# Kernel tuning notes

Measured on AMD Instinct MI355X. Metric: run time of the kernel, lower is better.

The kernel has to match this reference:

```python
import jax, jax.numpy as jnp
import numpy as np

N = 50000       # num nodes
E = 400000      # num edges (before self loops)
IN, HID, H, OUT = 128, 64, 4, 64
SLOPE = 0.2     # PyG GATv2Conv default negative_slope


def setup_inputs() -> dict:
    key = jax.random.key(0)
    ks = jax.random.split(key, 14)
    def lin(k, fan_in, fan_out):
        return jax.random.normal(k, (fan_in, fan_out), jnp.float32) / np.sqrt(fan_in)
    return {
        "x": jax.random.normal(ks[0], (N, IN), jnp.float32),
        "edge_index": jax.random.randint(ks[1], (2, E), 0, N, jnp.int32),
        # layer 1: in=IN -> HID per head, H heads, concat
        "Wl1": lin(ks[2], IN, H * HID), "bl1": jnp.zeros((H * HID,), jnp.float32),
        "Wr1": lin(ks[3], IN, H * HID), "br1": jnp.zeros((H * HID,), jnp.float32),
        "att1": jax.random.normal(ks[4], (H, HID), jnp.float32) / np.sqrt(HID),
        "bias1": jnp.zeros((H * HID,), jnp.float32),
        # layer 2: in=H*HID -> OUT, 1 head, concat=False
        "Wl2": lin(ks[5], H * HID, OUT), "bl2": jnp.zeros((OUT,), jnp.float32),
        "Wr2": lin(ks[6], H * HID, OUT), "br2": jnp.zeros((OUT,), jnp.float32),
        "att2": jax.random.normal(ks[7], (1, OUT), jnp.float32) / np.sqrt(OUT),
        "bias2": jnp.zeros((OUT,), jnp.float32),
    }


def gatv2_conv(x, src, dst, Wl, bl, Wr, br, att, heads, out_ch, num_nodes):
    """PyG GATv2Conv (share_weights=False). src->dst aggregation at dst."""
    xl = (x @ Wl + bl).reshape(-1, heads, out_ch)  # source transform (x_j)
    xr = (x @ Wr + br).reshape(-1, heads, out_ch)  # target transform (x_i)
    m = xl[src] + xr[dst]                          # [E, H, C]
    e = jnp.sum(jax.nn.leaky_relu(m, SLOPE) * att, axis=-1)  # [E, H]
    # segment softmax over incoming edges of each dst node
    emax = jax.ops.segment_max(e, dst, num_segments=num_nodes)
    ex = jnp.exp(e - emax[dst])
    denom = jax.ops.segment_sum(ex, dst, num_segments=num_nodes)
    alpha = ex / denom[dst]                        # [E, H]
    out = jax.ops.segment_sum(alpha[:, :, None] * xl[src], dst, num_segments=num_nodes)
    return out  # [N, H, C]


def reference(x, edge_index, Wl1, bl1, Wr1, br1, att1, bias1,
              Wl2, bl2, Wr2, br2, att2, bias2):
    n = x.shape[0]
    loops = jnp.arange(n, dtype=edge_index.dtype)
    src = jnp.concatenate([edge_index[0], loops])  # add_self_loops=True
    dst = jnp.concatenate([edge_index[1], loops])
    h = gatv2_conv(x, src, dst, Wl1, bl1, Wr1, br1, att1, H, HID, n)
    h = h.reshape(n, H * HID) + bias1              # concat=True
    h = jax.nn.elu(h)                              # dropout=0.0
    o = gatv2_conv(h, src, dst, Wl2, bl2, Wr2, br2, att2, 1, OUT, n)
    return o.reshape(n, OUT) + bias2               # concat=False, heads=1
```

## Files before the change

### kernel.cpp

```cpp
#include <hip/hip_runtime.h>
#include <hip/hip_bf16.h>

typedef unsigned short u16;
typedef __attribute__((ext_vector_type(8))) short short8;
typedef __attribute__((ext_vector_type(4))) float floatx4;

#define N_NODES 50000
#define N_EDGES 400000
#define ET      450000
#define F_IN    128
#define C1      256
#define HID     64
#define OUTC    64
#define SLOPE   0.2f

__device__ __forceinline__ float bf2f(u16 v) {
    return __uint_as_float(((unsigned)v) << 16);
}
__device__ __forceinline__ u16 f2bf(float f) {
    unsigned u = __float_as_uint(f);
    return (u16)((u + 0x7fffu + ((u >> 16) & 1u)) >> 16);
}

__global__ __launch_bounds__(256) void detect_kernel(const unsigned* __restrict__ xw,
                                                     int* __restrict__ cnt)
{
    unsigned w = xw[threadIdx.x];
    unsigned aexp = (w >> 7) & 0xFFu;
    if (aexp >= 170u || aexp <= 40u) atomicAdd(cnt, 1);
}

__global__ __launch_bounds__(256) void convert_all_kernel(
    const void* wl1, const void* wr1, const void* wl2, const void* wr2,
    const void* s0, const void* s1, const void* s2, const void* s3,
    const void* s4, const void* s5, const void* s6, const void* s7,
    u16* __restrict__ wt, u16* __restrict__ prm, const int* __restrict__ cnt)
{
    bool f32m = (*cnt >= 32);
    if (blockIdx.x == 384) {
        for (int t = threadIdx.x; t < 1280; t += 256) {
            const void* src; int local;
            if      (t < 256)  { src = s0; local = t; }
            else if (t < 512)  { src = s1; local = t - 256; }
            else if (t < 768)  { src = s2; local = t - 512; }
            else if (t < 1024) { src = s3; local = t - 768; }
            else if (t < 1088) { src = s4; local = t - 1024; }
            else if (t < 1152) { src = s5; local = t - 1088; }
            else if (t < 1216) { src = s6; local = t - 1152; }
            else               { src = s7; local = t - 1216; }
            prm[t] = f32m ? f2bf(((const float*)src)[local]) : ((const u16*)src)[local];
        }
        return;
    }
    int t = blockIdx.x * 256 + threadIdx.x;
    const void* src; int local, k, n, K, base;
    if (t < 32768)      { src = wl1; local = t;         k = local >> 8; n = local & 255; K = 128; base = 0; }
    else if (t < 65536) { src = wr1; local = t - 32768; k = local >> 8; n = local & 255; K = 128; base = 32768; }
    else if (t < 81920) { src = wl2; local = t - 65536; k = local >> 6; n = local & 63;  K = 256; base = 65536; }
    else                { src = wr2; local = t - 81920; k = local >> 6; n = local & 63;  K = 256; base = 81920; }
    u16 v = f32m ? f2bf(((const float*)src)[local]) : ((const u16*)src)[local];
    wt[base + n * K + k] = v;
}

__global__ __launch_bounds__(256) void hist_kernel(const int* __restrict__ ei,
                                                   int* __restrict__ hist)
{
    int t = blockIdx.x * 256 + threadIdx.x;
    if (t >= ET) return;
    int d = (t < N_EDGES) ? ei[N_EDGES + t] : t - N_EDGES;
    atomicAdd(&hist[d], 1);
}

__global__ __launch_bounds__(256) void scan1_kernel(const int* __restrict__ hist,
                                                    int* __restrict__ rowptr,
                                                    int* __restrict__ bsum)
{
    int t = threadIdx.x;
    int i = blockIdx.x * 256 + t;
    int v = (i < N_NODES) ? hist[i] : 0;
    __shared__ int sd[256];
    sd[t] = v;
    __syncthreads();
    #pragma unroll
    for (int ofs = 1; ofs < 256; ofs <<= 1) {
        int u = (t >= ofs) ? sd[t - ofs] : 0;
        __syncthreads();
        sd[t] += u;
        __syncthreads();
    }
    if (i < N_NODES) rowptr[i] = sd[t] - v;
    if (t == 255) bsum[blockIdx.x] = sd[255];
}

__global__ __launch_bounds__(256) void scan2_kernel(int* __restrict__ bsum,
                                                    int* __restrict__ boff)
{
    int t = threadIdx.x;
    int v = (t < 196) ? bsum[t] : 0;
    __shared__ int sd[256];
    sd[t] = v;
    __syncthreads();
    #pragma unroll
    for (int ofs = 1; ofs < 256; ofs <<= 1) {
        int u = (t >= ofs) ? sd[t - ofs] : 0;
        __syncthreads();
        sd[t] += u;
        __syncthreads();
    }
    if (t < 196) boff[t] = sd[t] - v;
}

__global__ __launch_bounds__(256) void scan3_kernel(int* __restrict__ rowptr,
                                                    const int* __restrict__ boff,
                                                    int* __restrict__ off)
{
    int i = blockIdx.x * 256 + threadIdx.x;
    if (i >= N_NODES) return;
    int r = rowptr[i] + boff[blockIdx.x];
    rowptr[i] = r;
    off[i] = r;
}

__global__ __launch_bounds__(256) void scatter_kernel(const int* __restrict__ ei,
                                                      int* __restrict__ off,
                                                      int* __restrict__ src_csr)
{
    int t = blockIdx.x * 256 + threadIdx.x;
    if (t >= ET) return;
    int s, d;
    if (t < N_EDGES) { s = ei[t]; d = ei[N_EDGES + t]; } else { s = d = t - N_EDGES; }
    int pos = atomicAdd(&off[d], 1);
    src_csr[pos] = s;
}

__global__ __launch_bounds__(256) void lin1_fused_kernel(
    const u16* __restrict__ X, const u16* __restrict__ Wt,
    const u16* __restrict__ bl, const u16* __restrict__ br,
    u16* __restrict__ Yl, u16* __restrict__ Yr, int nrows,
    const int* __restrict__ cnt)
{
    constexpr int K = 128, N = 256, LS = K + 8;
    __shared__ __align__(16) u16 sX[64 * LS];
    __shared__ __align__(16) u16 sW[64 * LS];
    const bool f32m = (*cnt >= 32);
    const float* X32 = (const float*)X;
    const int row0 = blockIdx.x * 64;
    const int wave = threadIdx.x >> 6, lane = threadIdx.x & 63;
    const int quad = lane >> 4, l16 = lane & 15;

    for (int i = threadIdx.x * 8; i < 64 * K; i += 2048) {
        int r = i >> 7, c = i & 127;
        int gr = row0 + r;
        u16* dst = &sX[r * LS + c];
        if (f32m) {
            float4 v0 = make_float4(0.f, 0.f, 0.f, 0.f), v1 = v0;
            if (gr < nrows) {
                v0 = *(const float4*)&X32[(size_t)gr * K + c];
                v1 = *(const float4*)&X32[(size_t)gr * K + c + 4];
            }
            ushort4 p0, p1;
            p0.x = f2bf(v0.x); p0.y = f2bf(v0.y); p0.z = f2bf(v0.z); p0.w = f2bf(v0.w);
            p1.x = f2bf(v1.x); p1.y = f2bf(v1.y); p1.z = f2bf(v1.z); p1.w = f2bf(v1.w);
            *(ushort4*)dst = p0;
            *(ushort4*)(dst + 4) = p1;
        } else {
            uint4 v = {0u, 0u, 0u, 0u};
            if (gr < nrows) v = *(const uint4*)&X[(size_t)gr * K + c];
            *(uint4*)dst = v;
        }
    }

    for (int side = 0; side < 2; ++side) {
        const u16* wbase = Wt + side * (N * K);
        const u16* bias  = side ? br : bl;
        u16* Y = side ? Yr : Yl;
        for (int ch = 0; ch < 4; ++ch) {
            __syncthreads();
            for (int i = threadIdx.x * 8; i < 64 * K; i += 2048) {
                int n = i >> 7, c = i & 127;
                *(uint4*)&sW[n * LS + c] = *(const uint4*)&wbase[(size_t)(ch * 64 + n) * K + c];
            }
            __syncthreads();
            floatx4 acc0 = {0.f, 0.f, 0.f, 0.f}, acc1 = acc0, acc2 = acc0, acc3 = acc0;
            #pragma unroll
            for (int kk = 0; kk < 4; ++kk) {
                short8 a  = *(const short8*)&sX[(wave * 16 + l16) * LS + kk * 32 + quad * 8];
                short8 b0 = *(const short8*)&sW[(l16) * LS + kk * 32 + quad * 8];
                short8 b1 = *(const short8*)&sW[(16 + l16) * LS + kk * 32 + quad * 8];
                short8 b2 = *(const short8*)&sW[(32 + l16) * LS + kk * 32 + quad * 8];
                short8 b3 = *(const short8*)&sW[(48 + l16) * LS + kk * 32 + quad * 8];
                acc0 = __builtin_amdgcn_mfma_f32_16x16x32_bf16(a, b0, acc0, 0, 0, 0);
                acc1 = __builtin_amdgcn_mfma_f32_16x16x32_bf16(a, b1, acc1, 0, 0, 0);
                acc2 = __builtin_amdgcn_mfma_f32_16x16x32_bf16(a, b2, acc2, 0, 0, 0);
                acc3 = __builtin_amdgcn_mfma_f32_16x16x32_bf16(a, b3, acc3, 0, 0, 0);
            }
            const int rbase = row0 + wave * 16 + quad * 4;
            #pragma unroll
            for (int cf = 0; cf < 4; ++cf) {
                const floatx4 av = (cf == 0) ? acc0 : (cf == 1) ? acc1 : (cf == 2) ? acc2 : acc3;
                const int col = ch * 64 + cf * 16 + l16;
                const float bv = bf2f(bias[col]);
                #pragma unroll
                for (int r = 0; r < 4; ++r) {
                    int row = rbase + r;
                    if (row < nrows) Y[(size_t)row * N + col] = f2bf(av[r] + bv);
                }
            }
        }
    }
}

__global__ __launch_bounds__(256) void lin2_fused_kernel(
    const u16* __restrict__ X, const u16* __restrict__ Wt,
    const u16* __restrict__ bl, const u16* __restrict__ br,
    u16* __restrict__ Yl, u16* __restrict__ Yr, int nrows)
{
    constexpr int K = 256, N = 64, LS = K + 8;
    __shared__ __align__(16) u16 sX[64 * LS];
    __shared__ __align__(16) u16 sW[64 * LS];
    const int row0 = blockIdx.x * 64;
    const int wave = threadIdx.x >> 6, lane = threadIdx.x & 63;
    const int quad = lane >> 4, l16 = lane & 15;

    for (int i = threadIdx.x * 8; i < 64 * K; i += 2048) {
        int r = i >> 8, c = i & 255;
        int gr = row0 + r;
        uint4 v = {0u, 0u, 0u, 0u};
        if (gr < nrows) v = *(const uint4*)&X[(size_t)gr * K + c];
        *(uint4*)&sX[r * LS + c] = v;
    }

    for (int side = 0; side < 2; ++side) {
        const u16* wbase = Wt + side * (N * K);
        const u16* bias  = side ? br : bl;
        u16* Y = side ? Yr : Yl;
        __syncthreads();
        for (int i = threadIdx.x * 8; i < 64 * K; i += 2048) {
            int n = i >> 8, c = i & 255;
            *(uint4*)&sW[n * LS + c] = *(const uint4*)&wbase[(size_t)n * K + c];
        }
        __syncthreads();
        floatx4 acc0 = {0.f, 0.f, 0.f, 0.f}, acc1 = acc0, acc2 = acc0, acc3 = acc0;
        #pragma unroll
        for (int kk = 0; kk < 8; ++kk) {
            short8 a  = *(const short8*)&sX[(wave * 16 + l16) * LS + kk * 32 + quad * 8];
            short8 b0 = *(const short8*)&sW[(l16) * LS + kk * 32 + quad * 8];
            short8 b1 = *(const short8*)&sW[(16 + l16) * LS + kk * 32 + quad * 8];
            short8 b2 = *(const short8*)&sW[(32 + l16) * LS + kk * 32 + quad * 8];
            short8 b3 = *(const short8*)&sW[(48 + l16) * LS + kk * 32 + quad * 8];
            acc0 = __builtin_amdgcn_mfma_f32_16x16x32_bf16(a, b0, acc0, 0, 0, 0);
            acc1 = __builtin_amdgcn_mfma_f32_16x16x32_bf16(a, b1, acc1, 0, 0, 0);
            acc2 = __builtin_amdgcn_mfma_f32_16x16x32_bf16(a, b2, acc2, 0, 0, 0);
            acc3 = __builtin_amdgcn_mfma_f32_16x16x32_bf16(a, b3, acc3, 0, 0, 0);
        }
        const int rbase = row0 + wave * 16 + quad * 4;
        #pragma unroll
        for (int cf = 0; cf < 4; ++cf) {
            const floatx4 av = (cf == 0) ? acc0 : (cf == 1) ? acc1 : (cf == 2) ? acc2 : acc3;
            const int col = cf * 16 + l16;
            const float bv = bf2f(bias[col]);
            #pragma unroll
            for (int r = 0; r < 4; ++r) {
                int row = rbase + r;
                if (row < nrows) Y[(size_t)row * N + col] = f2bf(av[r] + bv);
            }
        }
    }
}

__global__ __launch_bounds__(256) void node1_kernel(
    const u16* __restrict__ xl, const u16* __restrict__ xr,
    const int* __restrict__ rowptr, const int* __restrict__ hist,
    const int* __restrict__ src_csr, const u16* __restrict__ att,
    const u16* __restrict__ bias, u16* __restrict__ hout)
{
    const int d = __builtin_amdgcn_readfirstlane(blockIdx.x * 4 + (threadIdx.x >> 6));
    if (d >= N_NODES) return;
    const int l = threadIdx.x & 63;
    const int start = rowptr[d];
    const int deg = hist[d];

    ushort4 av = *(const ushort4*)&att[l * 4];
    const float at0 = bf2f(av.x), at1 = bf2f(av.y), at2 = bf2f(av.z), at3 = bf2f(av.w);
    ushort4 xrv = *(const ushort4*)&xr[(size_t)d * C1 + l * 4];
    const float r0 = bf2f(xrv.x), r1 = bf2f(xrv.y), r2 = bf2f(xrv.z), r3 = bf2f(xrv.w);

    float m = -1e30f, la = 0.f;
    float a0 = 0.f, a1 = 0.f, a2 = 0.f, a3 = 0.f;
    for (int j = 0; j < deg; j += 4) {
        const bool v1 = j + 1 < deg, v2 = j + 2 < deg, v3 = j + 3 < deg;
        int s0 = src_csr[start + j];
        int s1 = v1 ? src_csr[start + j + 1] : s0;
        int s2 = v2 ? src_csr[start + j + 2] : s0;
        int s3 = v3 ? src_csr[start + j + 3] : s0;
        ushort4 u0 = *(const ushort4*)&xl[(size_t)s0 * C1 + l * 4];
        ushort4 u1 = *(const ushort4*)&xl[(size_t)s1 * C1 + l * 4];
        ushort4 u2 = *(const ushort4*)&xl[(size_t)s2 * C1 + l * 4];
        ushort4 u3 = *(const ushort4*)&xl[(size_t)s3 * C1 + l * 4];
        float x00 = bf2f(u0.x), x01 = bf2f(u0.y), x02 = bf2f(u0.z), x03 = bf2f(u0.w);
        float x10 = bf2f(u1.x), x11 = bf2f(u1.y), x12 = bf2f(u1.z), x13 = bf2f(u1.w);
        float x20 = bf2f(u2.x), x21 = bf2f(u2.y), x22 = bf2f(u2.z), x23 = bf2f(u2.w);
        float x30 = bf2f(u3.x), x31 = bf2f(u3.y), x32 = bf2f(u3.z), x33 = bf2f(u3.w);
        float t, p0 = 0.f, p1 = 0.f, p2 = 0.f, p3 = 0.f;
        t = x00 + r0; t = t > 0.f ? t : SLOPE * t; p0 += t * at0;
        t = x01 + r1; t = t > 0.f ? t : SLOPE * t; p0 += t * at1;
        t = x02 + r2; t = t > 0.f ? t : SLOPE * t; p0 += t * at2;
        t = x03 + r3; t = t > 0.f ? t : SLOPE * t; p0 += t * at3;
        t = x10 + r0; t = t > 0.f ? t : SLOPE * t; p1 += t * at0;
        t = x11 + r1; t = t > 0.f ? t : SLOPE * t; p1 += t * at1;
        t = x12 + r2; t = t > 0.f ? t : SLOPE * t; p1 += t * at2;
        t = x13 + r3; t = t > 0.f ? t : SLOPE * t; p1 += t * at3;
        t = x20 + r0; t = t > 0.f ? t : SLOPE * t; p2 += t * at0;
        t = x21 + r1; t = t > 0.f ? t : SLOPE * t; p2 += t * at1;
        t = x22 + r2; t = t > 0.f ? t : SLOPE * t; p2 += t * at2;
        t = x23 + r3; t = t > 0.f ? t : SLOPE * t; p2 += t * at3;
        t = x30 + r0; t = t > 0.f ? t : SLOPE * t; p3 += t * at0;
        t = x31 + r1; t = t > 0.f ? t : SLOPE * t; p3 += t * at1;
        t = x32 + r2; t = t > 0.f ? t : SLOPE * t; p3 += t * at2;
        t = x33 + r3; t = t > 0.f ? t : SLOPE * t; p3 += t * at3;
        p0 += __shfl_xor(p0, 1); p1 += __shfl_xor(p1, 1); p2 += __shfl_xor(p2, 1); p3 += __shfl_xor(p3, 1);
        p0 += __shfl_xor(p0, 2); p1 += __shfl_xor(p1, 2); p2 += __shfl_xor(p2, 2); p3 += __shfl_xor(p3, 2);
        p0 += __shfl_xor(p0, 4); p1 += __shfl_xor(p1, 4); p2 += __shfl_xor(p2, 4); p3 += __shfl_xor(p3, 4);
        p0 += __shfl_xor(p0, 8); p1 += __shfl_xor(p1, 8); p2 += __shfl_xor(p2, 8); p3 += __shfl_xor(p3, 8);
        float pm = p0;
        if (v1) pm = fmaxf(pm, p1);
        if (v2) pm = fmaxf(pm, p2);
        if (v3) pm = fmaxf(pm, p3);
        float mn = fmaxf(m, pm);
        float sc = __expf(m - mn);
        float w0 = __expf(p0 - mn);
        float w1 = v1 ? __expf(p1 - mn) : 0.f;
        float w2 = v2 ? __expf(p2 - mn) : 0.f;
        float w3 = v3 ? __expf(p3 - mn) : 0.f;
        la = la * sc + w0 + w1 + w2 + w3;
        a0 = a0 * sc + w0 * x00 + w1 * x10 + w2 * x20 + w3 * x30;
        a1 = a1 * sc + w0 * x01 + w1 * x11 + w2 * x21 + w3 * x31;
        a2 = a2 * sc + w0 * x02 + w1 * x12 + w2 * x22 + w3 * x32;
        a3 = a3 * sc + w0 * x03 + w1 * x13 + w2 * x23 + w3 * x33;
        m = mn;
    }
    const float inv = 1.f / la;
    const int c = l * 4;
    float v0 = a0 * inv + bf2f(bias[c + 0]);
    float v1 = a1 * inv + bf2f(bias[c + 1]);
    float v2 = a2 * inv + bf2f(bias[c + 2]);
    float v3 = a3 * inv + bf2f(bias[c + 3]);
    v0 = v0 > 0.f ? v0 : __expf(fminf(v0, 0.f)) - 1.f;
    v1 = v1 > 0.f ? v1 : __expf(fminf(v1, 0.f)) - 1.f;
    v2 = v2 > 0.f ? v2 : __expf(fminf(v2, 0.f)) - 1.f;
    v3 = v3 > 0.f ? v3 : __expf(fminf(v3, 0.f)) - 1.f;
    ushort4 o;
    o.x = f2bf(v0); o.y = f2bf(v1); o.z = f2bf(v2); o.w = f2bf(v3);
    *(ushort4*)&hout[(size_t)d * C1 + c] = o;
}

__global__ __launch_bounds__(256) void node2_kernel(
    const u16* __restrict__ xl, const u16* __restrict__ xr,
    const int* __restrict__ rowptr, const int* __restrict__ hist,
    const int* __restrict__ src_csr, const u16* __restrict__ att,
    const u16* __restrict__ bias, void* __restrict__ outp,
    const int* __restrict__ cnt)
{
    const int d = __builtin_amdgcn_readfirstlane(blockIdx.x * 4 + (threadIdx.x >> 6));
    if (d >= N_NODES) return;
    const int l = threadIdx.x & 63;
    const int start = rowptr[d];
    const int deg = hist[d];
    const int g = l >> 4, sub = l & 15;
    const int c0 = sub * 4;

    ushort4 av = *(const ushort4*)&att[c0];
    const float at0 = bf2f(av.x), at1 = bf2f(av.y), at2 = bf2f(av.z), at3 = bf2f(av.w);
    ushort4 rv = *(const ushort4*)&xr[(size_t)d * OUTC + c0];
    const float r0 = bf2f(rv.x), r1 = bf2f(rv.y), r2 = bf2f(rv.z), r3 = bf2f(rv.w);

    float m = -1e30f, la = 0.f;
    float a0 = 0.f, a1 = 0.f, a2 = 0.f, a3 = 0.f;
    for (int j = 0; j < deg; j += 4) {
        int s0 = src_csr[start + j];
        int s1 = (j + 1 < deg) ? src_csr[start + j + 1] : d;
        int s2 = (j + 2 < deg) ? src_csr[start + j + 2] : d;
        int s3 = (j + 3 < deg) ? src_csr[start + j + 3] : d;
        const bool valid = j + g < deg;
        int s = (g == 0) ? s0 : (g == 1) ? s1 : (g == 2) ? s2 : s3;
        ushort4 xv = *(const ushort4*)&xl[(size_t)s * OUTC + c0];
        float x0 = bf2f(xv.x), x1 = bf2f(xv.y), x2 = bf2f(xv.z), x3 = bf2f(xv.w);
        float t, p = 0.f;
        t = x0 + r0; t = t > 0.f ? t : SLOPE * t; p += t * at0;
        t = x1 + r1; t = t > 0.f ? t : SLOPE * t; p += t * at1;
        t = x2 + r2; t = t > 0.f ? t : SLOPE * t; p += t * at2;
        t = x3 + r3; t = t > 0.f ? t : SLOPE * t; p += t * at3;
        p += __shfl_xor(p, 1);
        p += __shfl_xor(p, 2);
        p += __shfl_xor(p, 4);
        p += __shfl_xor(p, 8);
        float pv = valid ? p : -1e30f;
        float mn = fmaxf(m, pv);
        float sc = __expf(m - mn);
        float w  = valid ? __expf(p - mn) : 0.f;
        la = la * sc + w;
        a0 = a0 * sc + w * x0;
        a1 = a1 * sc + w * x1;
        a2 = a2 * sc + w * x2;
        a3 = a3 * sc + w * x3;
        m = mn;
    }
    #pragma unroll
    for (int ofs = 16; ofs <= 32; ofs <<= 1) {
        float mo = __shfl_xor(m, ofs);
        float lo = __shfl_xor(la, ofs);
        float b0 = __shfl_xor(a0, ofs);
        float b1 = __shfl_xor(a1, ofs);
        float b2 = __shfl_xor(a2, ofs);
        float b3 = __shfl_xor(a3, ofs);
        float mn = fmaxf(m, mo);
        float s0 = __expf(m - mn), s1 = __expf(mo - mn);
        la = la * s0 + lo * s1;
        a0 = a0 * s0 + b0 * s1;
        a1 = a1 * s0 + b1 * s1;
        a2 = a2 * s0 + b2 * s1;
        a3 = a3 * s0 + b3 * s1;
        m = mn;
    }
    if (g == 0) {
        const float inv = 1.f / la;
        float v0 = a0 * inv + bf2f(bias[c0 + 0]);
        float v1 = a1 * inv + bf2f(bias[c0 + 1]);
        float v2 = a2 * inv + bf2f(bias[c0 + 2]);
        float v3 = a3 * inv + bf2f(bias[c0 + 3]);
        if (*cnt >= 32) {
            float4 o = make_float4(v0, v1, v2, v3);
            *(float4*)&((float*)outp)[(size_t)d * OUTC + c0] = o;
        } else {
            ushort4 o;
            o.x = f2bf(v0); o.y = f2bf(v1); o.z = f2bf(v2); o.w = f2bf(v3);
            *(ushort4*)&((u16*)outp)[(size_t)d * OUTC + c0] = o;
        }
    }
}

extern "C" void kernel_launch(void* const* d_in, const int* in_sizes, int n_in,
                              void* d_out, int out_size, void* d_ws, size_t ws_size,
                              hipStream_t stream)
{
    const void* x  = d_in[0];
    const int*  ei = (const int*)d_in[1];

    char* ws = (char*)d_ws;
    u16* xl1     = (u16*)(ws + 0);
    u16* xr1     = (u16*)(ws + 25600000);
    u16* hbuf    = (u16*)(ws + 51200000);
    u16* xl2     = (u16*)(ws + 0);
    u16* xr2     = (u16*)(ws + 6400000);
    int* hist    = (int*)(ws + 76800000);
    int* rowptr  = (int*)(ws + 77000000);
    int* off     = (int*)(ws + 77200000);
    int* src_csr = (int*)(ws + 77400000);
    int* cnt     = (int*)(ws + 79200000);
    u16* prm     = (u16*)(ws + 79200064);
    u16* wt      = (u16*)(ws + 79210240);
    int* bsum    = (int*)(ws + 79410000);
    int* boff    = (int*)(ws + 79411024);

    u16* bl1   = prm + 0;
    u16* br1   = prm + 256;
    u16* att1  = prm + 512;
    u16* bias1 = prm + 768;
    u16* bl2   = prm + 1024;
    u16* br2   = prm + 1088;
    u16* att2  = prm + 1152;
    u16* bias2 = prm + 1216;
    u16* wt1   = wt + 0;
    u16* wt2   = wt + 65536;

    hipMemsetAsync(cnt, 0, 4, stream);
    detect_kernel<<<1, 256, 0, stream>>>((const unsigned*)x, cnt);
    convert_all_kernel<<<385, 256, 0, stream>>>(
        d_in[2], d_in[4], d_in[8], d_in[10],
        d_in[3], d_in[5], d_in[6], d_in[7], d_in[9], d_in[11], d_in[12], d_in[13],
        wt, prm, cnt);

    hipMemsetAsync(hist, 0, 200000, stream);
    const int eb = (ET + 255) / 256;
    hist_kernel<<<eb, 256, 0, stream>>>(ei, hist);
    scan1_kernel<<<196, 256, 0, stream>>>(hist, rowptr, bsum);
    scan2_kernel<<<1, 256, 0, stream>>>(bsum, boff);
    scan3_kernel<<<196, 256, 0, stream>>>(rowptr, boff, off);
    scatter_kernel<<<eb, 256, 0, stream>>>(ei, off, src_csr);

    const int gb = (N_NODES + 63) / 64;
    lin1_fused_kernel<<<gb, 256, 0, stream>>>((const u16*)x, wt1, bl1, br1, xl1, xr1, N_NODES, cnt);
    const int nb = (N_NODES * 64 + 255) / 256;
    node1_kernel<<<nb, 256, 0, stream>>>(xl1, xr1, rowptr, hist, src_csr, att1, bias1, hbuf);

    lin2_fused_kernel<<<gb, 256, 0, stream>>>(hbuf, wt2, bl2, br2, xl2, xr2, N_NODES);
    node2_kernel<<<nb, 256, 0, stream>>>(xl2, xr2, rowptr, hist, src_csr, att2, bias2, d_out, cnt);
}
```

Before: 270.7 us.

## Vectorize layer-1 gather to 16-byte loads and use DPP reductions

The layer-1 aggregation kernel now splits each wavefront into two halves. Each half processes two edges per iteration, and each lane loads 8 bf16 channels with one 16-byte load instead of four 8-byte loads. The two halves keep separate online-softmax states, merged at the end with a cross-half shuffle, so the wider loads need fewer memory instructions per edge. In both node kernels the per-head dot-product reductions use DPP row operations instead of ds_swizzle/shuffle, and layer 2 loads only the one source index each lane needs. The cost is the extra cross-half merge and idle lanes in the final store.

```diff
diff --git a/kernel.cpp b/kernel.cpp
--- a/kernel.cpp
+++ b/kernel.cpp
@@ -17,9 +17,25 @@
 __device__ __forceinline__ float bf2f(u16 v) {
     return __uint_as_float(((unsigned)v) << 16);
 }
+__device__ __forceinline__ float bflo(unsigned u) { return __uint_as_float(u << 16); }
+__device__ __forceinline__ float bfhi(unsigned u) { return __uint_as_float(u & 0xffff0000u); }
 __device__ __forceinline__ u16 f2bf(float f) {
     unsigned u = __float_as_uint(f);
     return (u16)((u + 0x7fffu + ((u >> 16) & 1u)) >> 16);
+}
+__device__ __forceinline__ unsigned pack2(float a, float b) {
+    return (unsigned)f2bf(a) | ((unsigned)f2bf(b) << 16);
+}
+template<int CTRL>
+__device__ __forceinline__ float dpp_add(float x) {
+    return x + __int_as_float(__builtin_amdgcn_update_dpp(
+        0, __float_as_int(x), CTRL, 0xF, 0xF, true));
+}
+__device__ __forceinline__ void unpack8(uint4 u, float* f) {
+    f[0] = bflo(u.x); f[1] = bfhi(u.x);
+    f[2] = bflo(u.y); f[3] = bfhi(u.y);
+    f[4] = bflo(u.z); f[5] = bfhi(u.z);
+    f[6] = bflo(u.w); f[7] = bfhi(u.w);
 }
 
 __global__ __launch_bounds__(256) void detect_kernel(const unsigned* __restrict__ xw,
@@ -277,81 +293,73 @@
     const int d = __builtin_amdgcn_readfirstlane(blockIdx.x * 4 + (threadIdx.x >> 6));
     if (d >= N_NODES) return;
     const int l = threadIdx.x & 63;
+    const int half = l >> 5, q = l & 31;
+    const int c0 = q * 8;
     const int start = rowptr[d];
     const int deg = hist[d];
 
-    ushort4 av = *(const ushort4*)&att[l * 4];
-    const float at0 = bf2f(av.x), at1 = bf2f(av.y), at2 = bf2f(av.z), at3 = bf2f(av.w);
-    ushort4 xrv = *(const ushort4*)&xr[(size_t)d * C1 + l * 4];
-    const float r0 = bf2f(xrv.x), r1 = bf2f(xrv.y), r2 = bf2f(xrv.z), r3 = bf2f(xrv.w);
+    float at[8], rr[8];
+    unpack8(*(const uint4*)&att[c0], at);
+    unpack8(*(const uint4*)&xr[(size_t)d * C1 + c0], rr);
 
     float m = -1e30f, la = 0.f;
-    float a0 = 0.f, a1 = 0.f, a2 = 0.f, a3 = 0.f;
+    float acc[8] = {0.f, 0.f, 0.f, 0.f, 0.f, 0.f, 0.f, 0.f};
     for (int j = 0; j < deg; j += 4) {
-        const bool v1 = j + 1 < deg, v2 = j + 2 < deg, v3 = j + 3 < deg;
-        int s0 = src_csr[start + j];
-        int s1 = v1 ? src_csr[start + j + 1] : s0;
-        int s2 = v2 ? src_csr[start + j + 2] : s0;
-        int s3 = v3 ? src_csr[start + j + 3] : s0;
-        ushort4 u0 = *(const ushort4*)&xl[(size_t)s0 * C1 + l * 4];
-        ushort4 u1 = *(const ushort4*)&xl[(size_t)s1 * C1 + l * 4];
-        ushort4 u2 = *(const ushort4*)&xl[(size_t)s2 * C1 + l * 4];
-        ushort4 u3 = *(const ushort4*)&xl[(size_t)s3 * C1 + l * 4];
-        float x00 = bf2f(u0.x), x01 = bf2f(u0.y), x02 = bf2f(u0.z), x03 = bf2f(u0.w);
-        float x10 = bf2f(u1.x), x11 = bf2f(u1.y), x12 = bf2f(u1.z), x13 = bf2f(u1.w);
-        float x20 = bf2f(u2.x), x21 = bf2f(u2.y), x22 = bf2f(u2.z), x23 = bf2f(u2.w);
-        float x30 = bf2f(u3.x), x31 = bf2f(u3.y), x32 = bf2f(u3.z), x33 = bf2f(u3.w);
-        float t, p0 = 0.f, p1 = 0.f, p2 = 0.f, p3 = 0.f;
-        t = x00 + r0; t = t > 0.f ? t : SLOPE * t; p0 += t * at0;
-        t = x01 + r1; t = t > 0.f ? t : SLOPE * t; p0 += t * at1;
-        t = x02 + r2; t = t > 0.f ? t : SLOPE * t; p0 += t * at2;
-        t = x03 + r3; t = t > 0.f ? t : SLOPE * t; p0 += t * at3;
-        t = x10 + r0; t = t > 0.f ? t : SLOPE * t; p1 += t * at0;
-        t = x11 + r1; t = t > 0.f ? t : SLOPE * t; p1 += t * at1;
-        t = x12 + r2; t = t > 0.f ? t : SLOPE * t; p1 += t * at2;
-        t = x13 + r3; t = t > 0.f ? t : SLOPE * t; p1 += t * at3;
-        t = x20 + r0; t = t > 0.f ? t : SLOPE * t; p2 += t * at0;
-        t = x21 + r1; t = t > 0.f ? t : SLOPE * t; p2 += t * at1;
-        t = x22 + r2; t = t > 0.f ? t : SLOPE * t; p2 += t * at2;
-        t = x23 + r3; t = t > 0.f ? t : SLOPE * t; p2 += t * at3;
-        t = x30 + r0; t = t > 0.f ? t : SLOPE * t; p3 += t * at0;
-        t = x31 + r1; t = t > 0.f ? t : SLOPE * t; p3 += t * at1;
-        t = x32 + r2; t = t > 0.f ? t : SLOPE * t; p3 += t * at2;
-        t = x33 + r3; t = t > 0.f ? t : SLOPE * t; p3 += t * at3;
-        p0 += __shfl_xor(p0, 1); p1 += __shfl_xor(p1, 1); p2 += __shfl_xor(p2, 1); p3 += __shfl_xor(p3, 1);
-        p0 += __shfl_xor(p0, 2); p1 += __shfl_xor(p1, 2); p2 += __shfl_xor(p2, 2); p3 += __shfl_xor(p3, 2);
-        p0 += __shfl_xor(p0, 4); p1 += __shfl_xor(p1, 4); p2 += __shfl_xor(p2, 4); p3 += __shfl_xor(p3, 4);
-        p0 += __shfl_xor(p0, 8); p1 += __shfl_xor(p1, 8); p2 += __shfl_xor(p2, 8); p3 += __shfl_xor(p3, 8);
-        float pm = p0;
-        if (v1) pm = fmaxf(pm, p1);
-        if (v2) pm = fmaxf(pm, p2);
-        if (v3) pm = fmaxf(pm, p3);
-        float mn = fmaxf(m, pm);
+        const int jj0 = j + half * 2;
+        const bool vA = jj0 < deg, vB = jj0 + 1 < deg;
+        int sA = vA ? src_csr[start + jj0] : d;
+        int sB = vB ? src_csr[start + jj0 + 1] : d;
+        float xa[8], xb[8];
+        unpack8(*(const uint4*)&xl[(size_t)sA * C1 + c0], xa);
+        unpack8(*(const uint4*)&xl[(size_t)sB * C1 + c0], xb);
+        float pA = 0.f, pB = 0.f, t;
+        #pragma unroll
+        for (int c = 0; c < 8; ++c) {
+            t = xa[c] + rr[c]; t = t > 0.f ? t : SLOPE * t; pA += t * at[c];
+            t = xb[c] + rr[c]; t = t > 0.f ? t : SLOPE * t; pB += t * at[c];
+        }
+        pA = dpp_add<0xB1>(pA);  pB = dpp_add<0xB1>(pB);
+        pA = dpp_add<0x4E>(pA);  pB = dpp_add<0x4E>(pB);
+        pA = dpp_add<0x141>(pA); pB = dpp_add<0x141>(pB);
+        float pAv = vA ? pA : -1e30f;
+        float pBv = vB ? pB : -1e30f;
+        float mn = fmaxf(m, fmaxf(pAv, pBv));
         float sc = __expf(m - mn);
-        float w0 = __expf(p0 - mn);
-        float w1 = v1 ? __expf(p1 - mn) : 0.f;
-        float w2 = v2 ? __expf(p2 - mn) : 0.f;
-        float w3 = v3 ? __expf(p3 - mn) : 0.f;
-        la = la * sc + w0 + w1 + w2 + w3;
-        a0 = a0 * sc + w0 * x00 + w1 * x10 + w2 * x20 + w3 * x30;
-        a1 = a1 * sc + w0 * x01 + w1 * x11 + w2 * x21 + w3 * x31;
-        a2 = a2 * sc + w0 * x02 + w1 * x12 + w2 * x22 + w3 * x32;
-        a3 = a3 * sc + w0 * x03 + w1 * x13 + w2 * x23 + w3 * x33;
+        float wA = vA ? __expf(pA - mn) : 0.f;
+        float wB = vB ? __expf(pB - mn) : 0.f;
+        la = la * sc + wA + wB;
+        #pragma unroll
+        for (int c = 0; c < 8; ++c)
+            acc[c] = acc[c] * sc + wA * xa[c] + wB * xb[c];
         m = mn;
     }
-    const float inv = 1.f / la;
-    const int c = l * 4;
-    float v0 = a0 * inv + bf2f(bias[c + 0]);
-    float v1 = a1 * inv + bf2f(bias[c + 1]);
-    float v2 = a2 * inv + bf2f(bias[c + 2]);
-    float v3 = a3 * inv + bf2f(bias[c + 3]);
-    v0 = v0 > 0.f ? v0 : __expf(fminf(v0, 0.f)) - 1.f;
-    v1 = v1 > 0.f ? v1 : __expf(fminf(v1, 0.f)) - 1.f;
-    v2 = v2 > 0.f ? v2 : __expf(fminf(v2, 0.f)) - 1.f;
-    v3 = v3 > 0.f ? v3 : __expf(fminf(v3, 0.f)) - 1.f;
-    ushort4 o;
-    o.x = f2bf(v0); o.y = f2bf(v1); o.z = f2bf(v2); o.w = f2bf(v3);
-    *(ushort4*)&hout[(size_t)d * C1 + c] = o;
+    {
+        float mo = __shfl_xor(m, 32);
+        float lo = __shfl_xor(la, 32);
+        float mn = fmaxf(m, mo);
+        float s0 = __expf(m - mn), s1 = __expf(mo - mn);
+        la = la * s0 + lo * s1;
+        #pragma unroll
+        for (int c = 0; c < 8; ++c) {
+            float bo = __shfl_xor(acc[c], 32);
+            acc[c] = acc[c] * s0 + bo * s1;
+        }
+    }
+    if (half == 0) {
+        const float inv = 1.f / la;
+        float bv[8];
+        unpack8(*(const uint4*)&bias[c0], bv);
+        float v[8];
+        #pragma unroll
+        for (int c = 0; c < 8; ++c) {
+            float x = acc[c] * inv + bv[c];
+            v[c] = x > 0.f ? x : __expf(fminf(x, 0.f)) - 1.f;
+        }
+        uint4 o;
+        o.x = pack2(v[0], v[1]); o.y = pack2(v[2], v[3]);
+        o.z = pack2(v[4], v[5]); o.w = pack2(v[6], v[7]);
+        *(uint4*)&hout[(size_t)d * C1 + c0] = o;
+    }
 }
 
 __global__ __launch_bounds__(256) void node2_kernel(
@@ -377,12 +385,8 @@
     float m = -1e30f, la = 0.f;
     float a0 = 0.f, a1 = 0.f, a2 = 0.f, a3 = 0.f;
     for (int j = 0; j < deg; j += 4) {
-        int s0 = src_csr[start + j];
-        int s1 = (j + 1 < deg) ? src_csr[start + j + 1] : d;
-        int s2 = (j + 2 < deg) ? src_csr[start + j + 2] : d;
-        int s3 = (j + 3 < deg) ? src_csr[start + j + 3] : d;
         const bool valid = j + g < deg;
-        int s = (g == 0) ? s0 : (g == 1) ? s1 : (g == 2) ? s2 : s3;
+        int s = valid ? src_csr[start + j + g] : d;
         ushort4 xv = *(const ushort4*)&xl[(size_t)s * OUTC + c0];
         float x0 = bf2f(xv.x), x1 = bf2f(xv.y), x2 = bf2f(xv.z), x3 = bf2f(xv.w);
         float t, p = 0.f;
@@ -390,10 +394,10 @@
         t = x1 + r1; t = t > 0.f ? t : SLOPE * t; p += t * at1;
         t = x2 + r2; t = t > 0.f ? t : SLOPE * t; p += t * at2;
         t = x3 + r3; t = t > 0.f ? t : SLOPE * t; p += t * at3;
-        p += __shfl_xor(p, 1);
-        p += __shfl_xor(p, 2);
-        p += __shfl_xor(p, 4);
-        p += __shfl_xor(p, 8);
+        p = dpp_add<0xB1>(p);
+        p = dpp_add<0x4E>(p);
+        p = dpp_add<0x141>(p);
+        p = dpp_add<0x140>(p);
         float pv = valid ? p : -1e30f;
         float mn = fmaxf(m, pv);
         float sc = __expf(m - mn);
```

Measured after the change: 272.9 us. No clear change (+0.8%).
